# Kernel tuning notes

Measured on AMD Instinct MI355X. Metric: run time of the kernel, lower is better.

The kernel has to match this reference:

```python
import jax, jax.numpy as jnp
import numpy as np
from functools import partial

OUT = 11  # out_channels of both MDLSTM layers
NDIR = 4  # Graves MDLSTM: 4 scan directions (2 per axis); height==1 so vertical neighbor is always the zero boundary state


def mdlstm(x, W, U, b):
    """Multi-directional LSTM over a height-1 strip.
    x: (B, Cin, 1, Wd); W: (4, Cin, 5*OUT); U: (4, OUT, 5*OUT); b: (4, 5*OUT)
    Gates per step: [i, f_w, f_h, o, a]. With height==1 the vertical cell state
    is the zero boundary, so the f_h branch contributes nothing.
    Returns (B, 4, OUT, 1, Wd).
    """
    B, Cin, _, Wd = x.shape
    xs = jnp.transpose(x[:, :, 0, :], (0, 2, 1))          # (B, Wd, Cin)
    xr = xs[:, ::-1, :]                                    # width-reversed
    xd = jnp.stack([xs, xr, xs, xr], axis=0)               # (4, B, Wd, Cin)
    # Precompute input contribution to all gates for every step.
    gx = jnp.einsum('dbwc,dcg->wdbg', xd, W) + b[None, :, None, :]  # (Wd,4,B,5*OUT)

    def step(carry, g_t):
        h, c = carry                                       # each (4, B, OUT)
        g = g_t + jnp.einsum('dbo,dog->dbg', h, U)         # (4, B, 5*OUT)
        i, f_w, f_h, o, a = jnp.split(g, 5, axis=-1)
        i = jax.nn.sigmoid(i)
        f_w = jax.nn.sigmoid(f_w)
        o = jax.nn.sigmoid(o)
        a = jnp.tanh(a)
        c_new = i * a + f_w * c                            # + sigmoid(f_h) * 0 (vertical boundary)
        h_new = o * jnp.tanh(c_new)
        return (h_new, c_new), h_new

    init = (jnp.zeros((NDIR, B, OUT), x.dtype), jnp.zeros((NDIR, B, OUT), x.dtype))
    _, hs = jax.lax.scan(step, init, gx)                   # (Wd, 4, B, OUT)
    h = jnp.transpose(hs, (2, 1, 3, 0))                    # (B, 4, OUT, Wd)
    # un-reverse the right-to-left directions
    h = h.at[:, 1].set(h[:, 1, :, ::-1]).at[:, 3].set(h[:, 3, :, ::-1])
    return h[:, :, :, None, :]                             # (B, 4, OUT, 1, Wd)


def setup_inputs() -> dict:
    key = jax.random.key(0)
    ks = jax.random.split(key, 7)
    B, H, Wd = 256, 32, 2048
    s = 0.1
    return {
        'x':  jax.random.normal(ks[0], (B, 1, H, Wd), jnp.float32),
        'W0': s * jax.random.normal(ks[1], (NDIR, 1,   5 * OUT), jnp.float32),
        'U0': s * jax.random.normal(ks[2], (NDIR, OUT, 5 * OUT), jnp.float32),
        'b0': jnp.zeros((NDIR, 5 * OUT), jnp.float32),
        'W1': s * jax.random.normal(ks[3], (NDIR, OUT, 5 * OUT), jnp.float32),
        'U1': s * jax.random.normal(ks[4], (NDIR, OUT, 5 * OUT), jnp.float32),
        'b1': jnp.zeros((NDIR, 5 * OUT), jnp.float32),
    }


def reference(x, W0, U0, b0, W1, U1, b1):
    x = x.sum(axis=2, keepdims=True)                       # (B, 1, 1, Wd)
    y = mdlstm(x, W0, U0, b0).sum(axis=1)                  # (B, 11, 1, Wd): sum over directions
    y = mdlstm(y, W1, U1, b1).sum(axis=1)                  # (B, 11, 1, Wd)
    return y[:, :, 0, :]                                   # (B, 11, Wd)
```

## Files before the change

### kernel.cpp

```cpp
#include <hip/hip_runtime.h>
#include <hip/hip_bf16.h>


#define NOUT 11
#define WD 2048
#define NB 256
#define ROW 12
#define ACCN (WD * ROW)
#define YROW 6
#define YPAD 12
#define YBFN (WD * YROW + 2 * YPAD)

#define NTHR 1024
#define NCK 16
#define CHUNK 128
#define WARM 40

typedef float f2 __attribute__((ext_vector_type(2)));
typedef float f4 __attribute__((ext_vector_type(4)));
typedef unsigned int u32;
typedef u32 u32x2 __attribute__((ext_vector_type(2)));
typedef __fp16 h2 __attribute__((ext_vector_type(2)));

#define LOG2E 1.4426950408889634f

union UH { u32 u; h2 h; };
__device__ __forceinline__ u32 h2u(h2 v) { UH x; x.h = v; return x.u; }
__device__ __forceinline__ h2 u2h(u32 v) { UH x; x.u = v; return x.h; }

template <int CTRL>
__device__ __forceinline__ float dppf(float v) {
  return __int_as_float(__builtin_amdgcn_update_dpp(
      __float_as_int(v), __float_as_int(v), CTRL, 0xF, 0xF, false));
}
__device__ __forceinline__ h2 rorh(h2 v) {
  return u2h((u32)__builtin_amdgcn_update_dpp(
      (int)h2u(v), (int)h2u(v), 0x122, 0xF, 0xF, false));
}
__device__ __forceinline__ float rcp_(float x) { return __builtin_amdgcn_rcpf(x); }
__device__ __forceinline__ float exp2_(float x) { return __builtin_amdgcn_exp2f(x); }
__device__ __forceinline__ float dot2(h2 a, h2 b, float c) {
  return __builtin_amdgcn_fdot2(a, b, c, false);
}

#define STEP(DOACC, ...)                                                       \
  do {                                                                         \
    const float hEv = dppf<0xA0>(hj);    \
    const float hOd = dppf<0xF5>(hj);  \
    h2 rv = __builtin_amdgcn_cvt_pkrtz(hEv, hOd);   \
    __VA_ARGS__                                                                \
    float gI = dot2(rv, UpI[0], giI);                                          \
    float gF = dot2(rv, UpF[0], giF);                                          \
    float gO = dot2(rv, UpO[0], giO);                                          \
    float gA = dot2(rv, UpA[0], giA);                                          \
    _Pragma("unroll")                                                          \
    for (int s = 1; s < 8; ++s) {                                              \
      rv = rorh(rv);                                                           \
      gI = dot2(rv, UpI[s], gI);                                               \
      gF = dot2(rv, UpF[s], gF);                                               \
      gO = dot2(rv, UpO[s], gO);                                               \
      gA = dot2(rv, UpA[s], gA);                                               \
    }                                                                          \
    const float sI = rcp_(1.0f + exp2_(gI));                                   \
    const float sF = rcp_(1.0f + exp2_(gF));                                   \
    const float sO = rcp_(1.0f + exp2_(gO));                                   \
    const float sA = rcp_(1.0f + exp2_(gA));                                   \
    const float taS = fmaf(-4.0f * LOG2E, sA, 2.0f * LOG2E);     \
    cpr = fmaf(sF, cpr, sI * taS);                      \
    const float r2t = rcp_(1.0f + exp2_(cpr));                  \
    const float sO2 = sO + sO;                                                 \
    hj = fmaf(sO2, r2t, -sO);                                 \
    if (DOACC && wr) atomicAdd(&acc[ao], hj);                                  \
    ao += ad;                                                                  \
  } while (0)

__global__ __launch_bounds__(NTHR, 1) void mdlstm_fused(
    const float* __restrict__ x, const float* __restrict__ W0,
    const float* __restrict__ U0, const float* __restrict__ b0,
    const float* __restrict__ W1, const float* __restrict__ U1,
    const float* __restrict__ b1, float* __restrict__ out) {
  __shared__ __align__(16) float acc[ACCN];
  __shared__ __align__(16) u32 ybf[YBFN];

  const int tid = threadIdx.x;
  const int b = blockIdx.x;
  float* xw = (float*)ybf;

  {
    const f4* xb4 = (const f4*)(x + (size_t)b * 32 * WD);
    f4* xw4 = (f4*)xw;
    for (int w = tid; w < WD / 4; w += NTHR) {
      f4 s = xb4[w];
#pragma unroll
      for (int h = 1; h < 32; ++h) s += xb4[h * (WD / 4) + w];
      xw4[w] = s;
    }
    f4* a4 = (f4*)acc;
    const f4 z = {0.f, 0.f, 0.f, 0.f};
    for (int i = tid; i < ACCN / 4; i += NTHR) a4[i] = z;
  }
  __syncthreads();

  const int lane = tid & 63;
  const int wv = tid >> 6;
  const int grp = lane >> 4;
  const int u = lane & 15;
  const int chain = wv * 4 + grp;
  const int d = chain & 3;
  const int ck = chain >> 2;
  const bool fwd = ((d & 1) == 0);
  const int base = ck * CHUNK;
  const bool real = (u <= 10);
  const bool wr = real;
  const bool ck0z = (ck == 0);
  const int colI = real ? u : 54;
  const int colF = real ? (11 + u) : 54;
  const int colO = real ? (33 + u) : 54;
  const int colA = real ? (44 + u) : 54;
  const float sclS = real ? -LOG2E : 0.f;
  const float sclA = real ? (-2.f * LOG2E) : 0.f;

  const int li = lane & 15;
  const int pv =
      __builtin_amdgcn_update_dpp(0, li, 0x122, 0xF, 0xF, false);
  const bool rplus = (pv == ((li + 2) & 15));
  const int p0 = li >> 1;

  const int p0pos = fwd ? (base - WARM) : (WD - 1 - base + WARM);
  const int xd = fwd ? 1 : -1;
  const int ad = fwd ? ROW : -ROW;
  const int qd = fwd ? 3 : -3;

  auto loadUrot = [&](const float* U, int col, float scl, h2* Up) {
#pragma unroll
    for (int s = 0; s < 8; ++s) {
      const int pr = rplus ? ((p0 + s) & 7) : ((p0 + 8 - s) & 7);
      const int r0 = 2 * pr, r1 = r0 + 1;
      const int rr0 = (r0 <= 10) ? r0 : 0;
      const int rr1 = (r1 <= 10) ? r1 : 0;
      float a = U[(d * NOUT + rr0) * 55 + col] * scl;
      float bb = U[(d * NOUT + rr1) * 55 + col] * scl;
      a = (r0 <= 10) ? a : 0.f;
      bb = (r1 <= 10) ? bb : 0.f;
      Up[s] = __builtin_amdgcn_cvt_pkrtz(a, bb);
    }
  };
  auto loadW = [&](const float* U, int col, float scl, h2* Up) {
    float uv[12];
#pragma unroll
    for (int s = 0; s < NOUT; ++s) uv[s] = U[(d * NOUT + s) * 55 + col] * scl;
    uv[11] = 0.f;
#pragma unroll
    for (int k = 0; k < 6; ++k)
      Up[k] = __builtin_amdgcn_cvt_pkrtz(uv[2 * k], uv[2 * k + 1]);
  };

  {
    h2 UpI[8], UpF[8], UpO[8], UpA[8];
    loadUrot(U0, colI, sclS, UpI);
    loadUrot(U0, colF, sclS, UpF);
    loadUrot(U0, colO, sclS, UpO);
    loadUrot(U0, colA, sclA, UpA);
    const float WcI = W0[d * 55 + colI] * sclS;
    const float WcF = W0[d * 55 + colF] * sclS;
    const float WcO = W0[d * 55 + colO] * sclS;
    const float WcA = W0[d * 55 + colA] * sclA;
    const float bcI = b0[d * 55 + colI] * sclS;
    const float bcF = b0[d * 55 + colF] * sclS;
    const float bcO = b0[d * 55 + colO] * sclS;
    const float bcA = b0[d * 55 + colA] * sclA;

    int xo = p0pos;
    int ao = p0pos * ROW + u;
    float hj = 0.f, cpr = 0.f;
    float gnI = 0.f, gnF = 0.f, gnO = 0.f, gnA = 0.f;
    const float xc = xw[xo & (WD - 1)];
    xo += xd;
    float giI = fmaf(xc, WcI, bcI);
    float giF = fmaf(xc, WcF, bcF);
    float giO = fmaf(xc, WcO, bcO);
    float giA = fmaf(xc, WcA, bcA);
    float xn = xw[xo & (WD - 1)];
    xo += xd;

#define PREP1                                                                  \
    const float xn2 = xw[xo & (WD - 1)];         \
    xo += xd;                                                                  \
    gnI = fmaf(xn, WcI, bcI);                             \
    gnF = fmaf(xn, WcF, bcF);                                                  \
    gnO = fmaf(xn, WcO, bcO);                                                  \
    gnA = fmaf(xn, WcA, bcA);                                                  \
    xn = xn2;

    for (int t = 0; t < WARM; t += 2) {
      STEP(0, PREP1);
      giI = gnI; giF = gnF; giO = gnO; giA = gnA;
      STEP(0, PREP1);
      giI = gnI; giF = gnF; giO = gnO; giA = gnA;
    }
    hj = ck0z ? 0.f : hj;
    cpr = ck0z ? 0.f : cpr;
    for (int t = 0; t < CHUNK; t += 2) {
      STEP(1, PREP1);
      giI = gnI; giF = gnF; giO = gnO; giA = gnA;
      STEP(1, PREP1);
      giI = gnI; giF = gnF; giO = gnO; giA = gnA;
    }
#undef PREP1
  }
  __syncthreads();

  {
    const f2* a2 = (const f2*)acc;
    for (int i = tid; i < WD * YROW; i += NTHR) {
      const f2 v = a2[i];
      ybf[YPAD + i] = h2u(__builtin_amdgcn_cvt_pkrtz(v.x, v.y));
    }
    if (tid < YPAD) {
      ybf[tid] = 0;
      ybf[WD * YROW + YPAD + tid] = 0;
    }
  }
  __syncthreads();
  {
    f4* a4 = (f4*)acc;
    const f4 z = {0.f, 0.f, 0.f, 0.f};
    for (int i = tid; i < ACCN / 4; i += NTHR) a4[i] = z;
  }
  __syncthreads();

  {
    h2 UpI[8], UpF[8], UpO[8], UpA[8];
    h2 WpI[6], WpF[6], WpO[6], WpA[6];
    loadUrot(U1, colI, sclS, UpI);
    loadUrot(U1, colF, sclS, UpF);
    loadUrot(U1, colO, sclS, UpO);
    loadUrot(U1, colA, sclA, UpA);
    loadW(W1, colI, sclS, WpI);
    loadW(W1, colF, sclS, WpF);
    loadW(W1, colO, sclS, WpO);
    loadW(W1, colA, sclA, WpA);
    const float bcI = b1[d * 55 + colI] * sclS;
    const float bcF = b1[d * 55 + colF] * sclS;
    const float bcO = b1[d * 55 + colO] * sclS;
    const float bcA = b1[d * 55 + colA] * sclA;

    const u32x2* yv = (const u32x2*)ybf;
    int q = 3 * p0pos + 6;

    auto GIc = [&](const h2* Wp, float bc, u32x2 r0, u32x2 r1,
                   u32x2 r2) -> float {
      float A = dot2(u2h(r0.x), Wp[0], bc);
      A = dot2(u2h(r0.y), Wp[1], A);
      A = dot2(u2h(r1.x), Wp[2], A);
      A = dot2(u2h(r1.y), Wp[3], A);
      A = dot2(u2h(r2.x), Wp[4], A);
      A = dot2(u2h(r2.y), Wp[5], A);
      return A;
    };

    u32x2 c0 = yv[q];
    u32x2 c1 = yv[q + 1];
    u32x2 c2 = yv[q + 2];
    q += qd;
    u32x2 pr0 = yv[q];
    u32x2 pr1 = yv[q + 1];
    u32x2 pr2 = yv[q + 2];
    q += qd;

    float giI = GIc(WpI, bcI, c0, c1, c2);
    float giF = GIc(WpF, bcF, c0, c1, c2);
    float giO = GIc(WpO, bcO, c0, c1, c2);
    float giA = GIc(WpA, bcA, c0, c1, c2);

    int ao = p0pos * ROW + u;
    float hj = 0.f, cpr = 0.f;
    float gnI = 0.f, gnF = 0.f, gnO = 0.f, gnA = 0.f;

#define PREP2                                                                  \
    const u32x2 n0 = yv[q];                  \
    const u32x2 n1 = yv[q + 1];                                                \
    const u32x2 n2 = yv[q + 2];                                                \
    q += qd;                                                                   \
    gnI = GIc(WpI, bcI, pr0, pr1, pr2);                   \
    gnF = GIc(WpF, bcF, pr0, pr1, pr2);                                        \
    gnO = GIc(WpO, bcO, pr0, pr1, pr2);                                        \
    gnA = GIc(WpA, bcA, pr0, pr1, pr2);                                        \
    pr0 = n0;                                                                  \
    pr1 = n1;                                                                  \
    pr2 = n2;

    for (int t = 0; t < WARM; t += 2) {
      STEP(0, PREP2);
      giI = gnI; giF = gnF; giO = gnO; giA = gnA;
      STEP(0, PREP2);
      giI = gnI; giF = gnF; giO = gnO; giA = gnA;
    }
    hj = ck0z ? 0.f : hj;
    cpr = ck0z ? 0.f : cpr;
    for (int t = 0; t < CHUNK; t += 2) {
      STEP(1, PREP2);
      giI = gnI; giF = gnF; giO = gnO; giA = gnA;
      STEP(1, PREP2);
      giI = gnI; giF = gnF; giO = gnO; giA = gnA;
    }
#undef PREP2
  }
  __syncthreads();

  float* ob = out + (size_t)b * (NOUT * WD);
  for (int i = tid; i < NOUT * WD; i += NTHR) {
    const int jj = i >> 11;
    const int w = i & (WD - 1);
    ob[i] = acc[w * ROW + jj];
  }
}

extern "C" void kernel_launch(void* const* d_in, const int* in_sizes, int n_in,
                              void* d_out, int out_size, void* d_ws,
                              size_t ws_size, hipStream_t stream) {
  const float* x  = (const float*)d_in[0];
  const float* W0 = (const float*)d_in[1];
  const float* U0 = (const float*)d_in[2];
  const float* b0 = (const float*)d_in[3];
  const float* W1 = (const float*)d_in[4];
  const float* U1 = (const float*)d_in[5];
  const float* b1 = (const float*)d_in[6];
  float* out = (float*)d_out;

  mdlstm_fused<<<NB, NTHR, 0, stream>>>(x, W0, U0, b0, W1, U1, b1, out);
}
```

Before: 404.0 us.

## Interleave two independent chunk recurrences per wave and halve block threads

Each wave now runs two independent width chunks (ck and ck+8) of the same direction in lockstep, interleaving their DPP broadcasts, dot products and transcendental cell updates. The block shrinks from 1024 to 512 threads. The aim is to hide the serial latency of each recurrence step with instruction-level parallelism instead of more waves. The cost is roughly doubled register pressure per thread and fewer waves available to hide LDS and atomic latency.

```diff
diff --git a/kernel.cpp b/kernel.cpp
--- a/kernel.cpp
+++ b/kernel.cpp
@@ -11,7 +11,7 @@
 #define YPAD 12
 #define YBFN (WD * YROW + 2 * YPAD)
 
-#define NTHR 1024
+#define NTHR 512
 #define NCK 16
 #define CHUNK 128
 #define WARM 40
@@ -43,36 +43,68 @@
   return __builtin_amdgcn_fdot2(a, b, c, false);
 }
 
-#define STEP(DOACC, ...)                                                       \
-  do {                                                                         \
-    const float hEv = dppf<0xA0>(hj);    \
-    const float hOd = dppf<0xF5>(hj);  \
-    h2 rv = __builtin_amdgcn_cvt_pkrtz(hEv, hOd);   \
-    __VA_ARGS__                                                                \
-    float gI = dot2(rv, UpI[0], giI);                                          \
-    float gF = dot2(rv, UpF[0], giF);                                          \
-    float gO = dot2(rv, UpO[0], giO);                                          \
-    float gA = dot2(rv, UpA[0], giA);                                          \
+#define DIST(S)                                                                \
+    const float hEv##S = dppf<0xA0>(hj##S);                                    \
+    const float hOd##S = dppf<0xF5>(hj##S);                                    \
+    h2 rv##S = __builtin_amdgcn_cvt_pkrtz(hEv##S, hOd##S);
+
+#define DOTS(S)                                                                \
+    float gI##S = dot2(rv##S, UpI[0], giI##S);                                 \
+    float gF##S = dot2(rv##S, UpF[0], giF##S);                                 \
+    float gO##S = dot2(rv##S, UpO[0], giO##S);                                 \
+    float gA##S = dot2(rv##S, UpA[0], giA##S);                                 \
     _Pragma("unroll")                                                          \
     for (int s = 1; s < 8; ++s) {                                              \
-      rv = rorh(rv);                                                           \
-      gI = dot2(rv, UpI[s], gI);                                               \
-      gF = dot2(rv, UpF[s], gF);                                               \
-      gO = dot2(rv, UpO[s], gO);                                               \
-      gA = dot2(rv, UpA[s], gA);                                               \
-    }                                                                          \
-    const float sI = rcp_(1.0f + exp2_(gI));                                   \
-    const float sF = rcp_(1.0f + exp2_(gF));                                   \
-    const float sO = rcp_(1.0f + exp2_(gO));                                   \
-    const float sA = rcp_(1.0f + exp2_(gA));                                   \
-    const float taS = fmaf(-4.0f * LOG2E, sA, 2.0f * LOG2E);     \
-    cpr = fmaf(sF, cpr, sI * taS);                      \
-    const float r2t = rcp_(1.0f + exp2_(cpr));                  \
-    const float sO2 = sO + sO;                                                 \
-    hj = fmaf(sO2, r2t, -sO);                                 \
-    if (DOACC && wr) atomicAdd(&acc[ao], hj);                                  \
-    ao += ad;                                                                  \
-  } while (0)
+      rv##S = rorh(rv##S);                                                     \
+      gI##S = dot2(rv##S, UpI[s], gI##S);                                      \
+      gF##S = dot2(rv##S, UpF[s], gF##S);                                      \
+      gO##S = dot2(rv##S, UpO[s], gO##S);                                      \
+      gA##S = dot2(rv##S, UpA[s], gA##S);                                      \
+    }
+
+#define CELL(S, DOACC)                                                         \
+    const float sI##S = rcp_(1.0f + exp2_(gI##S));                             \
+    const float sF##S = rcp_(1.0f + exp2_(gF##S));                             \
+    const float sO##S = rcp_(1.0f + exp2_(gO##S));                             \
+    const float sA##S = rcp_(1.0f + exp2_(gA##S));                             \
+    const float taS##S = fmaf(-4.0f * LOG2E, sA##S, 2.0f * LOG2E);             \
+    cpr##S = fmaf(sF##S, cpr##S, sI##S * taS##S);                              \
+    const float r2t##S = rcp_(1.0f + exp2_(cpr##S));                           \
+    const float sO2##S = sO##S + sO##S;                                        \
+    hj##S = fmaf(sO2##S, r2t##S, -sO##S);                                      \
+    if (DOACC && wr) atomicAdd(&acc[ao##S], hj##S);                            \
+    ao##S += ad;
+
+#define COPY(S)                                                                \
+    giI##S = gnI##S; giF##S = gnF##S; giO##S = gnO##S; giA##S = gnA##S;
+
+#define L1PREP(S)                                                              \
+    const float xn2##S = xw[xo##S & (WD - 1)];                                 \
+    xo##S += xd;                                                               \
+    gnI##S = fmaf(xn##S, WcI, bcI);                                            \
+    gnF##S = fmaf(xn##S, WcF, bcF);                                            \
+    gnO##S = fmaf(xn##S, WcO, bcO);                                            \
+    gnA##S = fmaf(xn##S, WcA, bcA);                                            \
+    xn##S = xn2##S;
+
+#define L2PREP(S)                                                              \
+    const u32x2 n0##S = yv[q##S];                                              \
+    const u32x2 n1##S = yv[q##S + 1];                                          \
+    const u32x2 n2##S = yv[q##S + 2];                                          \
+    q##S += qd;                                                                \
+    gnI##S = GIc(WpI, bcI, pr0##S, pr1##S, pr2##S);                            \
+    gnF##S = GIc(WpF, bcF, pr0##S, pr1##S, pr2##S);                            \
+    gnO##S = GIc(WpO, bcO, pr0##S, pr1##S, pr2##S);                            \
+    gnA##S = GIc(WpA, bcA, pr0##S, pr1##S, pr2##S);                            \
+    pr0##S = n0##S; pr1##S = n1##S; pr2##S = n2##S;
+
+#define L1STEP(DOACC)                                                          \
+    { DIST(A) DIST(B) L1PREP(A) L1PREP(B) DOTS(A) DOTS(B)                      \
+      CELL(A, DOACC) CELL(B, DOACC) COPY(A) COPY(B) }
+
+#define L2STEP(DOACC)                                                          \
+    { DIST(A) DIST(B) L2PREP(A) L2PREP(B) DOTS(A) DOTS(B)                      \
+      CELL(A, DOACC) CELL(B, DOACC) COPY(A) COPY(B) }
 
 __global__ __launch_bounds__(NTHR, 1) void mdlstm_fused(
     const float* __restrict__ x, const float* __restrict__ W0,
@@ -105,14 +137,13 @@
   const int wv = tid >> 6;
   const int grp = lane >> 4;
   const int u = lane & 15;
-  const int chain = wv * 4 + grp;
-  const int d = chain & 3;
-  const int ck = chain >> 2;
+  const int d = grp;
+  const int ckA = wv;
+  const int ckB = wv + 8;
   const bool fwd = ((d & 1) == 0);
-  const int base = ck * CHUNK;
   const bool real = (u <= 10);
   const bool wr = real;
-  const bool ck0z = (ck == 0);
+  const bool ck0zA = (wv == 0);
   const int colI = real ? u : 54;
   const int colF = real ? (11 + u) : 54;
   const int colO = real ? (33 + u) : 54;
@@ -126,7 +157,10 @@
   const bool rplus = (pv == ((li + 2) & 15));
   const int p0 = li >> 1;
 
-  const int p0pos = fwd ? (base - WARM) : (WD - 1 - base + WARM);
+  const int baseA = ckA * CHUNK;
+  const int baseB = ckB * CHUNK;
+  const int p0A = fwd ? (baseA - WARM) : (WD - 1 - baseA + WARM);
+  const int p0B = fwd ? (baseB - WARM) : (WD - 1 - baseB + WARM);
   const int xd = fwd ? 1 : -1;
   const int ad = fwd ? ROW : -ROW;
   const int qd = fwd ? 3 : -3;
@@ -170,43 +204,32 @@
     const float bcO = b0[d * 55 + colO] * sclS;
     const float bcA = b0[d * 55 + colA] * sclA;
 
-    int xo = p0pos;
-    int ao = p0pos * ROW + u;
-    float hj = 0.f, cpr = 0.f;
-    float gnI = 0.f, gnF = 0.f, gnO = 0.f, gnA = 0.f;
-    const float xc = xw[xo & (WD - 1)];
-    xo += xd;
-    float giI = fmaf(xc, WcI, bcI);
-    float giF = fmaf(xc, WcF, bcF);
-    float giO = fmaf(xc, WcO, bcO);
-    float giA = fmaf(xc, WcA, bcA);
-    float xn = xw[xo & (WD - 1)];
-    xo += xd;
-
-#define PREP1                                                                  \
-    const float xn2 = xw[xo & (WD - 1)];         \
-    xo += xd;                                                                  \
-    gnI = fmaf(xn, WcI, bcI);                             \
-    gnF = fmaf(xn, WcF, bcF);                                                  \
-    gnO = fmaf(xn, WcO, bcO);                                                  \
-    gnA = fmaf(xn, WcA, bcA);                                                  \
-    xn = xn2;
+    int xoA = p0A, xoB = p0B;
+    int aoA = p0A * ROW + u, aoB = p0B * ROW + u;
+    float hjA = 0.f, cprA = 0.f, hjB = 0.f, cprB = 0.f;
+    float gnIA = 0.f, gnFA = 0.f, gnOA = 0.f, gnAA = 0.f;
+    float gnIB = 0.f, gnFB = 0.f, gnOB = 0.f, gnAB = 0.f;
+    const float xcA = xw[xoA & (WD - 1)];
+    const float xcB = xw[xoB & (WD - 1)];
+    xoA += xd; xoB += xd;
+    float giIA = fmaf(xcA, WcI, bcI), giFA = fmaf(xcA, WcF, bcF);
+    float giOA = fmaf(xcA, WcO, bcO), giAA = fmaf(xcA, WcA, bcA);
+    float giIB = fmaf(xcB, WcI, bcI), giFB = fmaf(xcB, WcF, bcF);
+    float giOB = fmaf(xcB, WcO, bcO), giAB = fmaf(xcB, WcA, bcA);
+    float xnA = xw[xoA & (WD - 1)];
+    float xnB = xw[xoB & (WD - 1)];
+    xoA += xd; xoB += xd;
 
     for (int t = 0; t < WARM; t += 2) {
-      STEP(0, PREP1);
-      giI = gnI; giF = gnF; giO = gnO; giA = gnA;
-      STEP(0, PREP1);
-      giI = gnI; giF = gnF; giO = gnO; giA = gnA;
-    }
-    hj = ck0z ? 0.f : hj;
-    cpr = ck0z ? 0.f : cpr;
+      L1STEP(0);
+      L1STEP(0);
+    }
+    hjA = ck0zA ? 0.f : hjA;
+    cprA = ck0zA ? 0.f : cprA;
     for (int t = 0; t < CHUNK; t += 2) {
-      STEP(1, PREP1);
-      giI = gnI; giF = gnF; giO = gnO; giA = gnA;
-      STEP(1, PREP1);
-      giI = gnI; giF = gnF; giO = gnO; giA = gnA;
-    }
-#undef PREP1
+      L1STEP(1);
+      L1STEP(1);
+    }
   }
   __syncthreads();
 
@@ -246,7 +269,8 @@
     const float bcA = b1[d * 55 + colA] * sclA;
 
     const u32x2* yv = (const u32x2*)ybf;
-    int q = 3 * p0pos + 6;
+    int qA = 3 * p0A + 6;
+    int qB = 3 * p0B + 6;
 
     auto GIc = [&](const h2* Wp, float bc, u32x2 r0, u32x2 r1,
                    u32x2 r2) -> float {
@@ -259,52 +283,37 @@
       return A;
     };
 
-    u32x2 c0 = yv[q];
-    u32x2 c1 = yv[q + 1];
-    u32x2 c2 = yv[q + 2];
-    q += qd;
-    u32x2 pr0 = yv[q];
-    u32x2 pr1 = yv[q + 1];
-    u32x2 pr2 = yv[q + 2];
-    q += qd;
-
-    float giI = GIc(WpI, bcI, c0, c1, c2);
-    float giF = GIc(WpF, bcF, c0, c1, c2);
-    float giO = GIc(WpO, bcO, c0, c1, c2);
-    float giA = GIc(WpA, bcA, c0, c1, c2);
-
-    int ao = p0pos * ROW + u;
-    float hj = 0.f, cpr = 0.f;
-    float gnI = 0.f, gnF = 0.f, gnO = 0.f, gnA = 0.f;
-
-#define PREP2                                                                  \
-    const u32x2 n0 = yv[q];                  \
-    const u32x2 n1 = yv[q + 1];                                                \
-    const u32x2 n2 = yv[q + 2];                                                \
-    q += qd;                                                                   \
-    gnI = GIc(WpI, bcI, pr0, pr1, pr2);                   \
-    gnF = GIc(WpF, bcF, pr0, pr1, pr2);                                        \
-    gnO = GIc(WpO, bcO, pr0, pr1, pr2);                                        \
-    gnA = GIc(WpA, bcA, pr0, pr1, pr2);                                        \
-    pr0 = n0;                                                                  \
-    pr1 = n1;                                                                  \
-    pr2 = n2;
+    u32x2 c0A = yv[qA], c1A = yv[qA + 1], c2A = yv[qA + 2];
+    u32x2 c0B = yv[qB], c1B = yv[qB + 1], c2B = yv[qB + 2];
+    qA += qd; qB += qd;
+    u32x2 pr0A = yv[qA], pr1A = yv[qA + 1], pr2A = yv[qA + 2];
+    u32x2 pr0B = yv[qB], pr1B = yv[qB + 1], pr2B = yv[qB + 2];
+    qA += qd; qB += qd;
+
+    float giIA = GIc(WpI, bcI, c0A, c1A, c2A);
+    float giFA = GIc(WpF, bcF, c0A, c1A, c2A);
+    float giOA = GIc(WpO, bcO, c0A, c1A, c2A);
+    float giAA = GIc(WpA, bcA, c0A, c1A, c2A);
+    float giIB = GIc(WpI, bcI, c0B, c1B, c2B);
+    float giFB = GIc(WpF, bcF, c0B, c1B, c2B);
+    float giOB = GIc(WpO, bcO, c0B, c1B, c2B);
+    float giAB = GIc(WpA, bcA, c0B, c1B, c2B);
+
+    int aoA = p0A * ROW + u, aoB = p0B * ROW + u;
+    float hjA = 0.f, cprA = 0.f, hjB = 0.f, cprB = 0.f;
+    float gnIA = 0.f, gnFA = 0.f, gnOA = 0.f, gnAA = 0.f;
+    float gnIB = 0.f, gnFB = 0.f, gnOB = 0.f, gnAB = 0.f;
 
     for (int t = 0; t < WARM; t += 2) {
-      STEP(0, PREP2);
-      giI = gnI; giF = gnF; giO = gnO; giA = gnA;
-      STEP(0, PREP2);
-      giI = gnI; giF = gnF; giO = gnO; giA = gnA;
-    }
-    hj = ck0z ? 0.f : hj;
-    cpr = ck0z ? 0.f : cpr;
+      L2STEP(0);
+      L2STEP(0);
+    }
+    hjA = ck0zA ? 0.f : hjA;
+    cprA = ck0zA ? 0.f : cprA;
     for (int t = 0; t < CHUNK; t += 2) {
-      STEP(1, PREP2);
-      giI = gnI; giF = gnF; giO = gnO; giA = gnA;
-      STEP(1, PREP2);
-      giI = gnI; giF = gnF; giO = gnO; giA = gnA;
-    }
-#undef PREP2
+      L2STEP(1);
+      L2STEP(1);
+    }
   }
   __syncthreads();
 
```

New measurement: 393.5 us. 1.03x faster.

## Split each batch row across two blocks with halo recompute for layer-2 inputs

Applied to the files above, without the earlier changes.

Each batch element is now processed by two 512-thread blocks, each owning half the width plus a halo region. Layer 1 is recomputed over an extended window so layer 2 has its inputs locally, and shared memory shrinks to the half-width footprint. The goal is more blocks per GPU (512 instead of 256) and better CU occupancy and overlap. In exchange, the halo steps at the edges of layer 1 are computed redundantly.

```diff
diff --git a/kernel.cpp b/kernel.cpp
--- a/kernel.cpp
+++ b/kernel.cpp
@@ -5,14 +5,19 @@
 #define NOUT 11
 #define WD 2048
 #define NB 256
+#define NBLK (NB * 2)
 #define ROW 12
-#define ACCN (WD * ROW)
+#define POS 1024
+#define AEXT 40
+#define XEXT 80
+#define ANPOS (POS + 2 * AEXT)
+#define XWN (POS + 2 * XEXT)
+#define ACCN (ANPOS * ROW)
 #define YROW 6
 #define YPAD 12
-#define YBFN (WD * YROW + 2 * YPAD)
-
-#define NTHR 1024
-#define NCK 16
+#define YBFN (ANPOS * YROW + 2 * YPAD)
+
+#define NTHR 512
 #define CHUNK 128
 #define WARM 40
 
@@ -43,11 +48,11 @@
   return __builtin_amdgcn_fdot2(a, b, c, false);
 }
 
-#define STEP(DOACC, ...)                                                       \
+#define STEP(WRP, ...)                                                         \
   do {                                                                         \
-    const float hEv = dppf<0xA0>(hj);    \
-    const float hOd = dppf<0xF5>(hj);  \
-    h2 rv = __builtin_amdgcn_cvt_pkrtz(hEv, hOd);   \
+    const float hEv = dppf<0xA0>(hj);                                          \
+    const float hOd = dppf<0xF5>(hj);                                          \
+    h2 rv = __builtin_amdgcn_cvt_pkrtz(hEv, hOd);                              \
     __VA_ARGS__                                                                \
     float gI = dot2(rv, UpI[0], giI);                                          \
     float gF = dot2(rv, UpF[0], giF);                                          \
@@ -65,14 +70,16 @@
     const float sF = rcp_(1.0f + exp2_(gF));                                   \
     const float sO = rcp_(1.0f + exp2_(gO));                                   \
     const float sA = rcp_(1.0f + exp2_(gA));                                   \
-    const float taS = fmaf(-4.0f * LOG2E, sA, 2.0f * LOG2E);     \
-    cpr = fmaf(sF, cpr, sI * taS);                      \
-    const float r2t = rcp_(1.0f + exp2_(cpr));                  \
+    const float taS = fmaf(-4.0f * LOG2E, sA, 2.0f * LOG2E);                   \
+    cpr = fmaf(sF, cpr, sI * taS);                                             \
+    const float r2t = rcp_(1.0f + exp2_(cpr));                                 \
     const float sO2 = sO + sO;                                                 \
-    hj = fmaf(sO2, r2t, -sO);                                 \
-    if (DOACC && wr) atomicAdd(&acc[ao], hj);                                  \
+    hj = fmaf(sO2, r2t, -sO);                                                  \
+    if (WRP) atomicAdd(&acc[ao], hj);                                          \
     ao += ad;                                                                  \
   } while (0)
+
+#define CP giI = gnI; giF = gnF; giO = gnO; giA = gnA;
 
 __global__ __launch_bounds__(NTHR, 1) void mdlstm_fused(
     const float* __restrict__ x, const float* __restrict__ W0,
@@ -83,17 +90,26 @@
   __shared__ __align__(16) u32 ybf[YBFN];
 
   const int tid = threadIdx.x;
-  const int b = blockIdx.x;
+  const int bid = blockIdx.x;
+  const int b = bid >> 1;
+  const int half = bid & 1;
+  const int POFF = half << 10;
+  const int XOFFR = POFF - XEXT;
+  const int AOFFR = POFF - AEXT;
   float* xw = (float*)ybf;
 
   {
-    const f4* xb4 = (const f4*)(x + (size_t)b * 32 * WD);
+    const float* xb = x + (size_t)b * 32 * WD;
     f4* xw4 = (f4*)xw;
-    for (int w = tid; w < WD / 4; w += NTHR) {
-      f4 s = xb4[w];
+    for (int i2 = tid; i2 < XWN / 4; i2 += NTHR) {
+      const int phys = XOFFR + 4 * i2;
+      f4 s = {0.f, 0.f, 0.f, 0.f};
+      if ((unsigned)phys < 2048u) {
+        s = *(const f4*)(xb + phys);
 #pragma unroll
-      for (int h = 1; h < 32; ++h) s += xb4[h * (WD / 4) + w];
-      xw4[w] = s;
+        for (int h = 1; h < 32; ++h) s += *(const f4*)(xb + h * WD + phys);
+      }
+      xw4[i2] = s;
     }
     f4* a4 = (f4*)acc;
     const f4 z = {0.f, 0.f, 0.f, 0.f};
@@ -103,16 +119,16 @@
 
   const int lane = tid & 63;
   const int wv = tid >> 6;
-  const int grp = lane >> 4;
+  const int d = lane >> 4;
   const int u = lane & 15;
-  const int chain = wv * 4 + grp;
-  const int d = chain & 3;
-  const int ck = chain >> 2;
+  const int ck = wv;
   const bool fwd = ((d & 1) == 0);
-  const int base = ck * CHUNK;
   const bool real = (u <= 10);
   const bool wr = real;
-  const bool ck0z = (ck == 0);
+  const bool outerG = (half == 0) ? fwd : !fwd;
+  const bool rz0 = (wv == 0) && outerG;
+  const bool wrm = wr && (wv == 0) && !outerG;
+  const bool wre = wr && outerG;
   const int colI = real ? u : 54;
   const int colF = real ? (11 + u) : 54;
   const int colO = real ? (33 + u) : 54;
@@ -121,15 +137,18 @@
   const float sclA = real ? (-2.f * LOG2E) : 0.f;
 
   const int li = lane & 15;
-  const int pv =
-      __builtin_amdgcn_update_dpp(0, li, 0x122, 0xF, 0xF, false);
+  const int pv = __builtin_amdgcn_update_dpp(0, li, 0x122, 0xF, 0xF, false);
   const bool rplus = (pv == ((li + 2) & 15));
   const int p0 = li >> 1;
 
-  const int p0pos = fwd ? (base - WARM) : (WD - 1 - base + WARM);
+  const int s0 = fwd ? (POFF + ck * CHUNK) : (POFF + POS - 1 - ck * CHUNK);
+  const int wl1 = (wv == 0) ? (WARM + AEXT) : WARM;
+  const int st1 = fwd ? (s0 - wl1) : (s0 + wl1);
+  const int st2 = fwd ? (s0 - WARM) : (s0 + WARM);
   const int xd = fwd ? 1 : -1;
   const int ad = fwd ? ROW : -ROW;
   const int qd = fwd ? 3 : -3;
+  const int pre = wl1 - WARM;
 
   auto loadUrot = [&](const float* U, int col, float scl, h2* Up) {
 #pragma unroll
@@ -170,41 +189,47 @@
     const float bcO = b0[d * 55 + colO] * sclS;
     const float bcA = b0[d * 55 + colA] * sclA;
 
-    int xo = p0pos;
-    int ao = p0pos * ROW + u;
+    int xo = st1 - XOFFR;
+    int ao = (st1 - AOFFR) * ROW + u;
     float hj = 0.f, cpr = 0.f;
     float gnI = 0.f, gnF = 0.f, gnO = 0.f, gnA = 0.f;
-    const float xc = xw[xo & (WD - 1)];
+    const float xc = xw[xo];
     xo += xd;
     float giI = fmaf(xc, WcI, bcI);
     float giF = fmaf(xc, WcF, bcF);
     float giO = fmaf(xc, WcO, bcO);
     float giA = fmaf(xc, WcA, bcA);
-    float xn = xw[xo & (WD - 1)];
+    float xn = xw[xo];
     xo += xd;
 
 #define PREP1                                                                  \
-    const float xn2 = xw[xo & (WD - 1)];         \
+    const float xn2 = xw[xo];                                                  \
     xo += xd;                                                                  \
-    gnI = fmaf(xn, WcI, bcI);                             \
+    gnI = fmaf(xn, WcI, bcI);                                                  \
     gnF = fmaf(xn, WcF, bcF);                                                  \
     gnO = fmaf(xn, WcO, bcO);                                                  \
     gnA = fmaf(xn, WcA, bcA);                                                  \
     xn = xn2;
 
+    for (int t = 0; t < pre; t += 2) {
+      STEP(false, PREP1); CP;
+      STEP(false, PREP1); CP;
+    }
     for (int t = 0; t < WARM; t += 2) {
-      STEP(0, PREP1);
-      giI = gnI; giF = gnF; giO = gnO; giA = gnA;
-      STEP(0, PREP1);
-      giI = gnI; giF = gnF; giO = gnO; giA = gnA;
-    }
-    hj = ck0z ? 0.f : hj;
-    cpr = ck0z ? 0.f : cpr;
+      STEP(wrm, PREP1); CP;
+      STEP(wrm, PREP1); CP;
+    }
+    hj = rz0 ? 0.f : hj;
+    cpr = rz0 ? 0.f : cpr;
     for (int t = 0; t < CHUNK; t += 2) {
-      STEP(1, PREP1);
-      giI = gnI; giF = gnF; giO = gnO; giA = gnA;
-      STEP(1, PREP1);
-      giI = gnI; giF = gnF; giO = gnO; giA = gnA;
+      STEP(wr, PREP1); CP;
+      STEP(wr, PREP1); CP;
+    }
+    if (wv == 7) {
+      for (int t = 0; t < AEXT; t += 2) {
+        STEP(wre, PREP1); CP;
+        STEP(wre, PREP1); CP;
+      }
     }
 #undef PREP1
   }
@@ -212,13 +237,13 @@
 
   {
     const f2* a2 = (const f2*)acc;
-    for (int i = tid; i < WD * YROW; i += NTHR) {
+    for (int i = tid; i < ANPOS * YROW; i += NTHR) {
       const f2 v = a2[i];
       ybf[YPAD + i] = h2u(__builtin_amdgcn_cvt_pkrtz(v.x, v.y));
     }
     if (tid < YPAD) {
       ybf[tid] = 0;
-      ybf[WD * YROW + YPAD + tid] = 0;
+      ybf[YPAD + ANPOS * YROW + tid] = 0;
     }
   }
   __syncthreads();
@@ -246,7 +271,7 @@
     const float bcA = b1[d * 55 + colA] * sclA;
 
     const u32x2* yv = (const u32x2*)ybf;
-    int q = 3 * p0pos + 6;
+    int q = 3 * (st2 - AOFFR) + 6;
 
     auto GIc = [&](const h2* Wp, float bc, u32x2 r0, u32x2 r1,
                    u32x2 r2) -> float {
@@ -259,13 +284,9 @@
       return A;
     };
 
-    u32x2 c0 = yv[q];
-    u32x2 c1 = yv[q + 1];
-    u32x2 c2 = yv[q + 2];
+    u32x2 c0 = yv[q], c1 = yv[q + 1], c2 = yv[q + 2];
     q += qd;
-    u32x2 pr0 = yv[q];
-    u32x2 pr1 = yv[q + 1];
-    u32x2 pr2 = yv[q + 2];
+    u32x2 pr0 = yv[q], pr1 = yv[q + 1], pr2 = yv[q + 2];
     q += qd;
 
     float giI = GIc(WpI, bcI, c0, c1, c2);
@@ -273,16 +294,16 @@
     float giO = GIc(WpO, bcO, c0, c1, c2);
     float giA = GIc(WpA, bcA, c0, c1, c2);
 
-    int ao = p0pos * ROW + u;
+    int ao = (st2 - AOFFR) * ROW + u;
     float hj = 0.f, cpr = 0.f;
     float gnI = 0.f, gnF = 0.f, gnO = 0.f, gnA = 0.f;
 
 #define PREP2                                                                  \
-    const u32x2 n0 = yv[q];                  \
+    const u32x2 n0 = yv[q];                                                    \
     const u32x2 n1 = yv[q + 1];                                                \
     const u32x2 n2 = yv[q + 2];                                                \
     q += qd;                                                                   \
-    gnI = GIc(WpI, bcI, pr0, pr1, pr2);                   \
+    gnI = GIc(WpI, bcI, pr0, pr1, pr2);                                        \
     gnF = GIc(WpF, bcF, pr0, pr1, pr2);                                        \
     gnO = GIc(WpO, bcO, pr0, pr1, pr2);                                        \
     gnA = GIc(WpA, bcA, pr0, pr1, pr2);                                        \
@@ -291,28 +312,24 @@
     pr2 = n2;
 
     for (int t = 0; t < WARM; t += 2) {
-      STEP(0, PREP2);
-      giI = gnI; giF = gnF; giO = gnO; giA = gnA;
-      STEP(0, PREP2);
-      giI = gnI; giF = gnF; giO = gnO; giA = gnA;
-    }
-    hj = ck0z ? 0.f : hj;
-    cpr = ck0z ? 0.f : cpr;
+      STEP(false, PREP2); CP;
+      STEP(false, PREP2); CP;
+    }
+    hj = rz0 ? 0.f : hj;
+    cpr = rz0 ? 0.f : cpr;
     for (int t = 0; t < CHUNK; t += 2) {
-      STEP(1, PREP2);
-      giI = gnI; giF = gnF; giO = gnO; giA = gnA;
-      STEP(1, PREP2);
-      giI = gnI; giF = gnF; giO = gnO; giA = gnA;
+      STEP(wr, PREP2); CP;
+      STEP(wr, PREP2); CP;
     }
 #undef PREP2
   }
   __syncthreads();
 
-  float* ob = out + (size_t)b * (NOUT * WD);
-  for (int i = tid; i < NOUT * WD; i += NTHR) {
-    const int jj = i >> 11;
-    const int w = i & (WD - 1);
-    ob[i] = acc[w * ROW + jj];
+  float* ob = out + (size_t)b * (NOUT * WD) + POFF;
+  for (int i = tid; i < NOUT * POS; i += NTHR) {
+    const int jj = i >> 10;
+    const int w = i & (POS - 1);
+    ob[jj * WD + w] = acc[(w + AEXT) * ROW + jj];
   }
 }
 
@@ -328,5 +345,5 @@
   const float* b1 = (const float*)d_in[6];
   float* out = (float*)d_out;
 
-  mdlstm_fused<<<NB, NTHR, 0, stream>>>(x, W0, U0, b0, W1, U1, b1, out);
-}
+  mdlstm_fused<<<NBLK, NTHR, 0, stream>>>(x, W0, U0, b0, W1, U1, b1, out);
+}
```

New measurement: 414.5 us. 1.03x slower.
